# Performance work log

Hardware: AMD Instinct MI355X
Metric: run time of the kernel (lower is better)

## Reference

```python
import jax, jax.numpy as jnp
import numpy as np

NUM_SEQS = 16
NUM_HEADS = 32
NUM_KV_HEADS = 8
HEAD_SIZE = 128
BLOCK_SIZE = 16
X = 8  # vectorized key-cache packing factor
MAX_CTX = 4096
MAX_BLOCKS = MAX_CTX // BLOCK_SIZE
NUM_BLOCKS = NUM_SEQS * MAX_BLOCKS
SCALE = 0.08838834764831845  # 1/sqrt(128)
NEG_INF = -1e30


def setup_inputs() -> dict:
    key0 = jax.random.key(0)
    ks = jax.random.split(key0, 5)
    query = jax.random.normal(ks[0], (NUM_SEQS, 1, NUM_HEADS * HEAD_SIZE), jnp.float32)
    key = jax.random.normal(ks[1], (NUM_SEQS, 1, NUM_KV_HEADS * HEAD_SIZE), jnp.float32)
    value = jax.random.normal(ks[2], (NUM_SEQS, 1, NUM_KV_HEADS * HEAD_SIZE), jnp.float32)
    key_cache = jax.random.normal(ks[3], (NUM_BLOCKS, NUM_KV_HEADS, HEAD_SIZE // X, BLOCK_SIZE, X), jnp.float32)
    value_cache = jax.random.normal(ks[4], (NUM_BLOCKS, NUM_KV_HEADS, HEAD_SIZE, BLOCK_SIZE), jnp.float32)
    rng = np.random.default_rng(0)
    block_tables = rng.permutation(NUM_BLOCKS).reshape(NUM_SEQS, MAX_BLOCKS).astype(np.int32)
    context_lens = rng.integers(256, MAX_CTX + 1, size=(NUM_SEQS,)).astype(np.int32)
    last = context_lens - 1
    slots = block_tables[np.arange(NUM_SEQS), last // BLOCK_SIZE].astype(np.int64) * BLOCK_SIZE + (last % BLOCK_SIZE)
    slot_mapping = slots.reshape(NUM_SEQS, 1)
    return {
        'query': query, 'key': key, 'value': value,
        'key_cache': key_cache, 'value_cache': value_cache,
        'block_tables': jnp.asarray(block_tables),
        'context_lens': jnp.asarray(context_lens),
        'slot_mapping': jnp.asarray(slot_mapping),
    }


def _paged_attention_decode(query, key, value, key_cache, value_cache, block_tables, context_lens, slot_mapping):
    S, L1, hidden = query.shape  # L1 == 1 (decode)
    nb, kvH, _, bs, x = key_cache.shape
    D = value_cache.shape[2]
    H = hidden // D
    G = H // kvH  # queries per kv head
    maxB = block_tables.shape[1]

    q = query.reshape(S, H, D)
    k_new = key.reshape(S, kvH, D)
    v_new = value.reshape(S, kvH, D)

    # --- reshape_and_cache: write new K/V into paged caches ---
    sm = slot_mapping.reshape(-1)
    blk, off = sm // bs, sm % bs
    key_cache = key_cache.at[blk, :, :, off, :].set(k_new.reshape(S, kvH, D // x, x))
    value_cache = value_cache.at[blk, :, :, off].set(v_new)

    # --- gather paged KV via block tables ---
    # key_cache [nb,kvH,D/x,bs,x] -> [nb,kvH,bs,D]
    kc = key_cache.transpose(0, 1, 3, 2, 4).reshape(nb, kvH, bs, D)
    vc = value_cache.transpose(0, 1, 3, 2)  # [nb,kvH,bs,D]
    keys = kc[block_tables].transpose(0, 1, 3, 2, 4).reshape(S, maxB * bs, kvH, D)
    vals = vc[block_tables].transpose(0, 1, 3, 2, 4).reshape(S, maxB * bs, kvH, D)

    # --- GQA attention with context-length masking ---
    qg = q.reshape(S, kvH, G, D)
    scores = jnp.einsum('skgd,slkd->skgl', qg, keys) * jnp.asarray(SCALE, q.dtype)
    valid = jnp.arange(maxB * bs)[None, :] < context_lens[:, None]  # [S,L]
    scores = jnp.where(valid[:, None, None, :], scores, NEG_INF)
    probs = jax.nn.softmax(scores, axis=-1)
    out = jnp.einsum('skgl,slkd->skgd', probs, vals)
    return out.reshape(S, 1, H * D)


def reference(query, key, value, key_cache, value_cache, block_tables, context_lens, slot_mapping):
    return _paged_attention_decode(query, key, value, key_cache, value_cache,
                                   block_tables, context_lens, slot_mapping)
```

## Files before the change

kernel.cpp:

```cpp
#include <hip/hip_runtime.h>

#define NSEQ   16
#define KVH    8
#define NG     4
#define HD     128
#define BS     16
#define MAXB   256
#define PART   256
#define NPART  16
#define NITEMS (NSEQ * KVH * NPART)
#define WPT    64
#define PSTRIDE 520
#define REC_BYTES ((size_t)NITEMS * PSTRIDE * 4)
#define SCALE_F 0.08838834764831845f
#define NWORKERS 1024

__global__ __launch_bounds__(256) void pa_partial_kernel(
    const float* __restrict__ query,
    const float* __restrict__ key,
    const float* __restrict__ value,
    const float* __restrict__ key_cache,
    const float* __restrict__ value_cache,
    const int*   __restrict__ block_tables,
    const int*   __restrict__ context_lens,
    float*       __restrict__ ws,
    unsigned int* __restrict__ counter)
{
    __shared__ float p_lds[4][NG][WPT];
    __shared__ float o_lds[4][NG * HD];
    __shared__ float ml_lds[4][8];
    __shared__ int   item_s;

    const int tid  = threadIdx.x;
    const int wv   = tid >> 6;
    const int lane = tid & 63;

    for (;;) {
        if (tid == 0) item_s = (int)atomicAdd(counter, 1u);
        __syncthreads();
        const int item = item_s;
        __syncthreads();
        if (item >= NITEMS) return;

        const int p   = item & (NPART - 1);
        const int kvh = (item >> 4) & (KVH - 1);
        const int s   = item >> 7;
        const int ctx = context_lens[s];
        const int t0  = p * PART;
        if (t0 >= ctx) continue;

        const int tw0  = t0 + wv * WPT;
        const bool wact = (tw0 < ctx);

        const float* q = query + ((size_t)s * KVH + kvh) * (NG * HD);

        float m_w = -1e30f;
        float l_w[NG] = {0.f, 0.f, 0.f, 0.f};

        if (wact) {
            const int t  = tw0 + lane;
            const int bt = block_tables[s * MAXB + (t >> 4)];
            const float* kb = key_cache + (size_t)bt * (KVH * HD * BS)
                                        + (size_t)kvh * (HD * BS) + (t & 15) * 8;

            float sc[NG] = {0.f, 0.f, 0.f, 0.f};
            #pragma unroll
            for (int j = 0; j < 16; ++j) {
                const float4 ka = *(const float4*)(kb + j * 128);
                const float4 kc = *(const float4*)(kb + j * 128 + 4);
                #pragma unroll
                for (int g = 0; g < NG; ++g) {
                    sc[g] += q[g * HD + j * 8 + 0] * ka.x + q[g * HD + j * 8 + 1] * ka.y
                           + q[g * HD + j * 8 + 2] * ka.z + q[g * HD + j * 8 + 3] * ka.w
                           + q[g * HD + j * 8 + 4] * kc.x + q[g * HD + j * 8 + 5] * kc.y
                           + q[g * HD + j * 8 + 6] * kc.z + q[g * HD + j * 8 + 7] * kc.w;
                }
            }

            if (t == ctx - 1) {
                const float4* kn4 = (const float4*)(key + ((size_t)s * KVH + kvh) * HD);
                float ns[NG] = {0.f, 0.f, 0.f, 0.f};
                #pragma unroll
                for (int c = 0; c < 32; ++c) {
                    const float4 k4 = kn4[c];
                    #pragma unroll
                    for (int g = 0; g < NG; ++g) {
                        ns[g] += q[g * HD + c * 4 + 0] * k4.x + q[g * HD + c * 4 + 1] * k4.y
                               + q[g * HD + c * 4 + 2] * k4.z + q[g * HD + c * 4 + 3] * k4.w;
                    }
                }
                #pragma unroll
                for (int g = 0; g < NG; ++g) sc[g] = ns[g];
            }

            float mv;
            if (t < ctx) {
                #pragma unroll
                for (int g = 0; g < NG; ++g) sc[g] *= SCALE_F;
                mv = fmaxf(fmaxf(sc[0], sc[1]), fmaxf(sc[2], sc[3]));
            } else {
                #pragma unroll
                for (int g = 0; g < NG; ++g) sc[g] = -1e30f;
                mv = -1e30f;
            }

            #pragma unroll
            for (int o = 32; o; o >>= 1) mv = fmaxf(mv, __shfl_xor(mv, o));
            m_w = mv;

            float pr[NG];
            #pragma unroll
            for (int g = 0; g < NG; ++g) {
                pr[g] = __expf(sc[g] - m_w);
                p_lds[wv][g][lane] = pr[g];
                l_w[g] = pr[g];
            }
            #pragma unroll
            for (int o = 32; o; o >>= 1) {
                l_w[0] += __shfl_xor(l_w[0], o);
                l_w[1] += __shfl_xor(l_w[1], o);
                l_w[2] += __shfl_xor(l_w[2], o);
                l_w[3] += __shfl_xor(l_w[3], o);
            }
        }

        if (lane == 0) {
            ml_lds[wv][0] = m_w;
            #pragma unroll
            for (int g = 0; g < NG; ++g) ml_lds[wv][1 + g] = l_w[g];
        }

        if (wact) {
            const int nbv = min(4, (ctx - tw0 + 15) >> 4);
            int btv[4];
            #pragma unroll
            for (int b = 0; b < 4; ++b)
                btv[b] = block_tables[s * MAXB + (tw0 >> 4) + b];

            const int tl = ctx - 1 - tw0;
            const float4* pl4 = (const float4*)&p_lds[wv][0][0];

            #pragma unroll 2
            for (int half = 0; half < 2; ++half) {
                const int d = lane + half * 64;
                float a[NG] = {0.f, 0.f, 0.f, 0.f};
                for (int b = 0; b < nbv; ++b) {
                    const float* vb = value_cache + (size_t)btv[b] * (KVH * HD * BS)
                                                  + (size_t)kvh * (HD * BS) + d * BS;
                    #pragma unroll
                    for (int c = 0; c < 4; ++c) {
                        const float4 v4 = *(const float4*)(vb + c * 4);
                        #pragma unroll
                        for (int g = 0; g < NG; ++g) {
                            const float4 pg = pl4[g * 16 + b * 4 + c];
                            a[g] += pg.x * v4.x + pg.y * v4.y + pg.z * v4.z + pg.w * v4.w;
                        }
                    }
                }
                if (tl >= 0 && tl < WPT) {
                    const int btn = block_tables[s * MAXB + ((ctx - 1) >> 4)];
                    const float vold = value_cache[(size_t)btn * (KVH * HD * BS)
                                                   + (size_t)kvh * (HD * BS) + d * BS + ((ctx - 1) & 15)];
                    const float vnew = value[((size_t)s * KVH + kvh) * HD + d];
                    const float dv = vnew - vold;
                    #pragma unroll
                    for (int g = 0; g < NG; ++g) a[g] += p_lds[wv][g][tl] * dv;
                }
                #pragma unroll
                for (int g = 0; g < NG; ++g) o_lds[wv][g * HD + d] = a[g];
            }
        } else {
            #pragma unroll
            for (int i = 0; i < 8; ++i) o_lds[wv][i * 64 + lane] = 0.f;
        }

        __syncthreads();

        const float m0 = ml_lds[0][0], m1 = ml_lds[1][0], m2 = ml_lds[2][0], m3 = ml_lds[3][0];
        const float M  = fmaxf(fmaxf(m0, m1), fmaxf(m2, m3));
        const float w0 = __expf(m0 - M), w1 = __expf(m1 - M);
        const float w2 = __expf(m2 - M), w3 = __expf(m3 - M);

        float* rec = ws + (size_t)item * PSTRIDE;
        #pragma unroll
        for (int r = 0; r < 2; ++r) {
            const int idx = tid + r * 256;
            rec[idx] = w0 * o_lds[0][idx] + w1 * o_lds[1][idx]
                     + w2 * o_lds[2][idx] + w3 * o_lds[3][idx];
        }
        if (tid < NG) {
            rec[512 + tid] = w0 * ml_lds[0][1 + tid] + w1 * ml_lds[1][1 + tid]
                           + w2 * ml_lds[2][1 + tid] + w3 * ml_lds[3][1 + tid];
        }
        if (tid == 4) rec[516] = M;
    }
}

__global__ __launch_bounds__(128) void pa_reduce_kernel(
    const float* __restrict__ ws,
    const int*   __restrict__ context_lens,
    float*       __restrict__ out)
{
    const int b    = blockIdx.x;
    const int g    = b & 3;
    const int pair = b >> 2;
    const int s    = pair >> 3;
    const int kvh  = pair & 7;
    const int ctx  = context_lens[s];
    const int np   = (ctx + PART - 1) / PART;

    const int d = threadIdx.x;
    const float* base = ws + (size_t)pair * NPART * PSTRIDE;

    float M = -1e30f;
    for (int p2 = 0; p2 < np; ++p2) M = fmaxf(M, base[p2 * PSTRIDE + 516]);

    float L = 0.f, acc = 0.f;
    for (int p2 = 0; p2 < np; ++p2) {
        const float* rec = base + p2 * PSTRIDE;
        const float w = __expf(rec[516] - M);
        L   += w * rec[512 + g];
        acc += w * rec[g * HD + d];
    }

    out[(size_t)s * (KVH * NG * HD) + (size_t)(kvh * NG + g) * HD + d] = acc / L;
}

extern "C" void kernel_launch(void* const* d_in, const int* in_sizes, int n_in,
                              void* d_out, int out_size, void* d_ws, size_t ws_size,
                              hipStream_t stream) {
    const float* query       = (const float*)d_in[0];
    const float* key         = (const float*)d_in[1];
    const float* value       = (const float*)d_in[2];
    const float* key_cache   = (const float*)d_in[3];
    const float* value_cache = (const float*)d_in[4];
    const int*   block_tables  = (const int*)d_in[5];
    const int*   context_lens  = (const int*)d_in[6];

    float* out = (float*)d_out;
    float* ws  = (float*)d_ws;
    unsigned int* counter = (unsigned int*)((char*)d_ws + REC_BYTES);

    hipMemsetAsync(counter, 0, sizeof(unsigned int), stream);
    pa_partial_kernel<<<NWORKERS, 256, 0, stream>>>(
        query, key, value, key_cache, value_cache, block_tables, context_lens, ws, counter);
    pa_reduce_kernel<<<NSEQ * KVH * NG, 128, 0, stream>>>(ws, context_lens, out);
}
```

Before: 85.02 us.

## Make each wavefront an independent worker processing 128-token chunks without block sync

Work items become per-wavefront chunks of 128 tokens, each wave grabbing its own item through a lane-0 atomic and broadcast, so the block-level barriers and the cross-wave LDS merge are gone. Each lane now handles two tokens in QK and two head-dim columns in PV, and writes its partial record straight to the workspace. The grid shrinks to 512 blocks, and the reduce kernel now merges up to 32 partials per head instead of 16. In exchange there are more atomics on the counter, more workspace traffic, and more work in the reduction.

After: 298.8 us. +251.4%, slower.

```diff
diff --git a/kernel.cpp b/kernel.cpp
--- a/kernel.cpp
+++ b/kernel.cpp
@@ -6,14 +6,13 @@
 #define HD     128
 #define BS     16
 #define MAXB   256
-#define PART   256
-#define NPART  16
-#define NITEMS (NSEQ * KVH * NPART)
-#define WPT    64
+#define WPT    128
+#define NCHUNK 32
+#define NITEMS (NSEQ * KVH * NCHUNK)
 #define PSTRIDE 520
 #define REC_BYTES ((size_t)NITEMS * PSTRIDE * 4)
 #define SCALE_F 0.08838834764831845f
-#define NWORKERS 1024
+#define NBLOCKS 512
 
 __global__ __launch_bounds__(256) void pa_partial_kernel(
     const float* __restrict__ query,
@@ -26,173 +25,167 @@
     float*       __restrict__ ws,
     unsigned int* __restrict__ counter)
 {
-    __shared__ float p_lds[4][NG][WPT];
-    __shared__ float o_lds[4][NG * HD];
-    __shared__ float ml_lds[4][8];
-    __shared__ int   item_s;
-
+    __shared__ float p_all[4][NG][WPT];
     const int tid  = threadIdx.x;
     const int wv   = tid >> 6;
     const int lane = tid & 63;
+    float* pw = &p_all[wv][0][0];
 
     for (;;) {
-        if (tid == 0) item_s = (int)atomicAdd(counter, 1u);
-        __syncthreads();
-        const int item = item_s;
-        __syncthreads();
+        int item;
+        if (lane == 0) item = (int)atomicAdd(counter, 1u);
+        item = __shfl(item, 0);
         if (item >= NITEMS) return;
 
-        const int p   = item & (NPART - 1);
-        const int kvh = (item >> 4) & (KVH - 1);
-        const int s   = item >> 7;
+        const int ck  = item & (NCHUNK - 1);
+        const int kvh = (item >> 5) & (KVH - 1);
+        const int s   = item >> 8;
         const int ctx = context_lens[s];
-        const int t0  = p * PART;
+        const int t0  = ck * WPT;
         if (t0 >= ctx) continue;
 
-        const int tw0  = t0 + wv * WPT;
-        const bool wact = (tw0 < ctx);
-
-        const float* q = query + ((size_t)s * KVH + kvh) * (NG * HD);
-
-        float m_w = -1e30f;
-        float l_w[NG] = {0.f, 0.f, 0.f, 0.f};
-
-        if (wact) {
-            const int t  = tw0 + lane;
-            const int bt = block_tables[s * MAXB + (t >> 4)];
-            const float* kb = key_cache + (size_t)bt * (KVH * HD * BS)
-                                        + (size_t)kvh * (HD * BS) + (t & 15) * 8;
-
-            float sc[NG] = {0.f, 0.f, 0.f, 0.f};
-            #pragma unroll
-            for (int j = 0; j < 16; ++j) {
-                const float4 ka = *(const float4*)(kb + j * 128);
-                const float4 kc = *(const float4*)(kb + j * 128 + 4);
+        const float*  q      = query + ((size_t)s * KVH + kvh) * (NG * HD);
+        const size_t  kvhoff = (size_t)kvh * (HD * BS);
+
+        const int tA  = t0 + lane;
+        const int tB  = t0 + 64 + lane;
+        const int btA = block_tables[s * MAXB + (tA >> 4)];
+        const int btB = block_tables[s * MAXB + (tB >> 4)];
+        const float* kbA = key_cache + (size_t)btA * (KVH * HD * BS) + kvhoff + (tA & 15) * 8;
+        const float* kbB = key_cache + (size_t)btB * (KVH * HD * BS) + kvhoff + (tB & 15) * 8;
+
+        float scA[NG] = {0.f, 0.f, 0.f, 0.f};
+        float scB[NG] = {0.f, 0.f, 0.f, 0.f};
+        #pragma unroll
+        for (int j = 0; j < 16; ++j) {
+            const float4 a0 = *(const float4*)(kbA + j * 128);
+            const float4 a1 = *(const float4*)(kbA + j * 128 + 4);
+            const float4 b0 = *(const float4*)(kbB + j * 128);
+            const float4 b1 = *(const float4*)(kbB + j * 128 + 4);
+            #pragma unroll
+            for (int g = 0; g < NG; ++g) {
+                const float* qg = q + g * HD + j * 8;
+                scA[g] += qg[0]*a0.x + qg[1]*a0.y + qg[2]*a0.z + qg[3]*a0.w
+                        + qg[4]*a1.x + qg[5]*a1.y + qg[6]*a1.z + qg[7]*a1.w;
+                scB[g] += qg[0]*b0.x + qg[1]*b0.y + qg[2]*b0.z + qg[3]*b0.w
+                        + qg[4]*b1.x + qg[5]*b1.y + qg[6]*b1.z + qg[7]*b1.w;
+            }
+        }
+
+        if (tA == ctx - 1) {
+            const float4* kn4 = (const float4*)(key + ((size_t)s * KVH + kvh) * HD);
+            float ns[NG] = {0.f, 0.f, 0.f, 0.f};
+            #pragma unroll
+            for (int c = 0; c < 32; ++c) {
+                const float4 k4 = kn4[c];
                 #pragma unroll
                 for (int g = 0; g < NG; ++g) {
-                    sc[g] += q[g * HD + j * 8 + 0] * ka.x + q[g * HD + j * 8 + 1] * ka.y
-                           + q[g * HD + j * 8 + 2] * ka.z + q[g * HD + j * 8 + 3] * ka.w
-                           + q[g * HD + j * 8 + 4] * kc.x + q[g * HD + j * 8 + 5] * kc.y
-                           + q[g * HD + j * 8 + 6] * kc.z + q[g * HD + j * 8 + 7] * kc.w;
+                    const float* qg = q + g * HD + c * 4;
+                    ns[g] += qg[0]*k4.x + qg[1]*k4.y + qg[2]*k4.z + qg[3]*k4.w;
                 }
             }
-
-            if (t == ctx - 1) {
-                const float4* kn4 = (const float4*)(key + ((size_t)s * KVH + kvh) * HD);
-                float ns[NG] = {0.f, 0.f, 0.f, 0.f};
+            #pragma unroll
+            for (int g = 0; g < NG; ++g) scA[g] = ns[g];
+        }
+        if (tB == ctx - 1) {
+            const float4* kn4 = (const float4*)(key + ((size_t)s * KVH + kvh) * HD);
+            float ns[NG] = {0.f, 0.f, 0.f, 0.f};
+            #pragma unroll
+            for (int c = 0; c < 32; ++c) {
+                const float4 k4 = kn4[c];
                 #pragma unroll
-                for (int c = 0; c < 32; ++c) {
-                    const float4 k4 = kn4[c];
-                    #pragma unroll
-                    for (int g = 0; g < NG; ++g) {
-                        ns[g] += q[g * HD + c * 4 + 0] * k4.x + q[g * HD + c * 4 + 1] * k4.y
-                               + q[g * HD + c * 4 + 2] * k4.z + q[g * HD + c * 4 + 3] * k4.w;
-                    }
+                for (int g = 0; g < NG; ++g) {
+                    const float* qg = q + g * HD + c * 4;
+                    ns[g] += qg[0]*k4.x + qg[1]*k4.y + qg[2]*k4.z + qg[3]*k4.w;
                 }
+            }
+            #pragma unroll
+            for (int g = 0; g < NG; ++g) scB[g] = ns[g];
+        }
+
+        float mv = -1e30f;
+        if (tA < ctx) {
+            #pragma unroll
+            for (int g = 0; g < NG; ++g) { scA[g] *= SCALE_F; mv = fmaxf(mv, scA[g]); }
+        } else {
+            #pragma unroll
+            for (int g = 0; g < NG; ++g) scA[g] = -1e30f;
+        }
+        if (tB < ctx) {
+            #pragma unroll
+            for (int g = 0; g < NG; ++g) { scB[g] *= SCALE_F; mv = fmaxf(mv, scB[g]); }
+        } else {
+            #pragma unroll
+            for (int g = 0; g < NG; ++g) scB[g] = -1e30f;
+        }
+        #pragma unroll
+        for (int o = 32; o; o >>= 1) mv = fmaxf(mv, __shfl_xor(mv, o));
+        const float m_w = mv;
+
+        float l[NG];
+        #pragma unroll
+        for (int g = 0; g < NG; ++g) {
+            const float pA = __expf(scA[g] - m_w);
+            const float pB = __expf(scB[g] - m_w);
+            pw[g * WPT + lane]      = pA;
+            pw[g * WPT + 64 + lane] = pB;
+            l[g] = pA + pB;
+        }
+        #pragma unroll
+        for (int o = 32; o; o >>= 1) {
+            l[0] += __shfl_xor(l[0], o);
+            l[1] += __shfl_xor(l[1], o);
+            l[2] += __shfl_xor(l[2], o);
+            l[3] += __shfl_xor(l[3], o);
+        }
+
+        const int nbv = min(8, (ctx - t0 + 15) >> 4);
+        float a0[NG] = {0.f, 0.f, 0.f, 0.f};
+        float a1[NG] = {0.f, 0.f, 0.f, 0.f};
+        const float4* pl4 = (const float4*)pw;
+        for (int b = 0; b < nbv; ++b) {
+            const int btv = block_tables[s * MAXB + (t0 >> 4) + b];
+            const float* vb = value_cache + (size_t)btv * (KVH * HD * BS) + kvhoff;
+            #pragma unroll
+            for (int c = 0; c < 4; ++c) {
+                const float4 v0 = *(const float4*)(vb + lane * BS + c * 4);
+                const float4 v1 = *(const float4*)(vb + (lane + 64) * BS + c * 4);
                 #pragma unroll
-                for (int g = 0; g < NG; ++g) sc[g] = ns[g];
-            }
-
-            float mv;
-            if (t < ctx) {
-                #pragma unroll
-                for (int g = 0; g < NG; ++g) sc[g] *= SCALE_F;
-                mv = fmaxf(fmaxf(sc[0], sc[1]), fmaxf(sc[2], sc[3]));
-            } else {
-                #pragma unroll
-                for (int g = 0; g < NG; ++g) sc[g] = -1e30f;
-                mv = -1e30f;
-            }
-
-            #pragma unroll
-            for (int o = 32; o; o >>= 1) mv = fmaxf(mv, __shfl_xor(mv, o));
-            m_w = mv;
-
-            float pr[NG];
+                for (int g = 0; g < NG; ++g) {
+                    const float4 pg = pl4[g * (WPT / 4) + b * 4 + c];
+                    a0[g] += pg.x*v0.x + pg.y*v0.y + pg.z*v0.z + pg.w*v0.w;
+                    a1[g] += pg.x*v1.x + pg.y*v1.y + pg.z*v1.z + pg.w*v1.w;
+                }
+            }
+        }
+
+        const int tl = ctx - 1 - t0;
+        if (tl >= 0 && tl < WPT) {
+            const int btn = block_tables[s * MAXB + ((ctx - 1) >> 4)];
+            const float* vbn = value_cache + (size_t)btn * (KVH * HD * BS) + kvhoff
+                             + ((ctx - 1) & 15);
+            const float dv0 = value[((size_t)s * KVH + kvh) * HD + lane]
+                            - vbn[lane * BS];
+            const float dv1 = value[((size_t)s * KVH + kvh) * HD + lane + 64]
+                            - vbn[(lane + 64) * BS];
             #pragma unroll
             for (int g = 0; g < NG; ++g) {
-                pr[g] = __expf(sc[g] - m_w);
-                p_lds[wv][g][lane] = pr[g];
-                l_w[g] = pr[g];
-            }
-            #pragma unroll
-            for (int o = 32; o; o >>= 1) {
-                l_w[0] += __shfl_xor(l_w[0], o);
-                l_w[1] += __shfl_xor(l_w[1], o);
-                l_w[2] += __shfl_xor(l_w[2], o);
-                l_w[3] += __shfl_xor(l_w[3], o);
-            }
-        }
-
+                a0[g] += pw[g * WPT + tl] * dv0;
+                a1[g] += pw[g * WPT + tl] * dv1;
+            }
+        }
+
+        float* rec = ws + (size_t)item * PSTRIDE;
+        #pragma unroll
+        for (int g = 0; g < NG; ++g) {
+            rec[g * HD + lane]      = a0[g];
+            rec[g * HD + 64 + lane] = a1[g];
+        }
         if (lane == 0) {
-            ml_lds[wv][0] = m_w;
-            #pragma unroll
-            for (int g = 0; g < NG; ++g) ml_lds[wv][1 + g] = l_w[g];
-        }
-
-        if (wact) {
-            const int nbv = min(4, (ctx - tw0 + 15) >> 4);
-            int btv[4];
-            #pragma unroll
-            for (int b = 0; b < 4; ++b)
-                btv[b] = block_tables[s * MAXB + (tw0 >> 4) + b];
-
-            const int tl = ctx - 1 - tw0;
-            const float4* pl4 = (const float4*)&p_lds[wv][0][0];
-
-            #pragma unroll 2
-            for (int half = 0; half < 2; ++half) {
-                const int d = lane + half * 64;
-                float a[NG] = {0.f, 0.f, 0.f, 0.f};
-                for (int b = 0; b < nbv; ++b) {
-                    const float* vb = value_cache + (size_t)btv[b] * (KVH * HD * BS)
-                                                  + (size_t)kvh * (HD * BS) + d * BS;
-                    #pragma unroll
-                    for (int c = 0; c < 4; ++c) {
-                        const float4 v4 = *(const float4*)(vb + c * 4);
-                        #pragma unroll
-                        for (int g = 0; g < NG; ++g) {
-                            const float4 pg = pl4[g * 16 + b * 4 + c];
-                            a[g] += pg.x * v4.x + pg.y * v4.y + pg.z * v4.z + pg.w * v4.w;
-                        }
-                    }
-                }
-                if (tl >= 0 && tl < WPT) {
-                    const int btn = block_tables[s * MAXB + ((ctx - 1) >> 4)];
-                    const float vold = value_cache[(size_t)btn * (KVH * HD * BS)
-                                                   + (size_t)kvh * (HD * BS) + d * BS + ((ctx - 1) & 15)];
-                    const float vnew = value[((size_t)s * KVH + kvh) * HD + d];
-                    const float dv = vnew - vold;
-                    #pragma unroll
-                    for (int g = 0; g < NG; ++g) a[g] += p_lds[wv][g][tl] * dv;
-                }
-                #pragma unroll
-                for (int g = 0; g < NG; ++g) o_lds[wv][g * HD + d] = a[g];
-            }
-        } else {
-            #pragma unroll
-            for (int i = 0; i < 8; ++i) o_lds[wv][i * 64 + lane] = 0.f;
-        }
-
-        __syncthreads();
-
-        const float m0 = ml_lds[0][0], m1 = ml_lds[1][0], m2 = ml_lds[2][0], m3 = ml_lds[3][0];
-        const float M  = fmaxf(fmaxf(m0, m1), fmaxf(m2, m3));
-        const float w0 = __expf(m0 - M), w1 = __expf(m1 - M);
-        const float w2 = __expf(m2 - M), w3 = __expf(m3 - M);
-
-        float* rec = ws + (size_t)item * PSTRIDE;
-        #pragma unroll
-        for (int r = 0; r < 2; ++r) {
-            const int idx = tid + r * 256;
-            rec[idx] = w0 * o_lds[0][idx] + w1 * o_lds[1][idx]
-                     + w2 * o_lds[2][idx] + w3 * o_lds[3][idx];
-        }
-        if (tid < NG) {
-            rec[512 + tid] = w0 * ml_lds[0][1 + tid] + w1 * ml_lds[1][1 + tid]
-                           + w2 * ml_lds[2][1 + tid] + w3 * ml_lds[3][1 + tid];
-        }
-        if (tid == 4) rec[516] = M;
+            #pragma unroll
+            for (int g = 0; g < NG; ++g) rec[512 + g] = l[g];
+            rec[516] = m_w;
+        }
     }
 }
 
@@ -207,10 +200,10 @@
     const int s    = pair >> 3;
     const int kvh  = pair & 7;
     const int ctx  = context_lens[s];
-    const int np   = (ctx + PART - 1) / PART;
+    const int np   = (ctx + WPT - 1) / WPT;
 
     const int d = threadIdx.x;
-    const float* base = ws + (size_t)pair * NPART * PSTRIDE;
+    const float* base = ws + (size_t)pair * NCHUNK * PSTRIDE;
 
     float M = -1e30f;
     for (int p2 = 0; p2 < np; ++p2) M = fmaxf(M, base[p2 * PSTRIDE + 516]);
@@ -242,7 +235,7 @@
     unsigned int* counter = (unsigned int*)((char*)d_ws + REC_BYTES);
 
     hipMemsetAsync(counter, 0, sizeof(unsigned int), stream);
-    pa_partial_kernel<<<NWORKERS, 256, 0, stream>>>(
+    pa_partial_kernel<<<NBLOCKS, 256, 0, stream>>>(
         query, key, value, key_cache, value_cache, block_tables, context_lens, ws, counter);
     pa_reduce_kernel<<<NSEQ * KVH * NG, 128, 0, stream>>>(ws, context_lens, out);
 }
```
